# Optimization experiments

Hardware: AMD Instinct MI355X
Metric: run time of the kernel (lower is better)

## Reference

```python
import jax, jax.numpy as jnp
import numpy as np

N, D, H, E = 50000, 128, 512, 500000

def setup_inputs() -> dict:
    key = jax.random.key(0)
    k1, k2, k3, k4 = jax.random.split(key, 4)
    z = jax.random.normal(k1, (N, D), dtype=jnp.float32)
    edge_index = jax.random.randint(k2, (2, E), 0, N, dtype=jnp.int64)
    # torch Linear weights: fc1 [H, 2D], fc2 [1, H]
    W1 = jax.random.normal(k3, (H, 2 * D), dtype=jnp.float32) * (1.0 / np.sqrt(2 * D))
    b1 = jnp.zeros((H,), dtype=jnp.float32)
    W2 = jax.random.normal(k4, (1, H), dtype=jnp.float32) * (1.0 / np.sqrt(H))
    b2 = jnp.zeros((1,), dtype=jnp.float32)
    return {"z": z, "edge_index": edge_index, "W1": W1, "b1": b1, "W2": W2, "b2": b2}

def reference(z, edge_index, W1, b1, W2, b2):
    # gather endpoints and concat along feature dim: [E, 2D]
    z_cat = jnp.concatenate([z[edge_index[0]], z[edge_index[1]]], axis=1)
    # dropout is identity at eval (drop_rate effectively 0 for the baseline)
    h = jax.nn.relu(jnp.einsum('ef,hf->eh', z_cat, W1) + b1)  # [E, H]
    y = (jnp.einsum('eh,oh->eo', h, W2) + b2).reshape(-1)     # [E]
    return y
```

## Files before the change

kernel.cpp:

```cpp
#include <hip/hip_runtime.h>


typedef __bf16 bf16x8 __attribute__((ext_vector_type(8)));
typedef float f32x4  __attribute__((ext_vector_type(4)));
typedef float f32x16 __attribute__((ext_vector_type(16)));

__device__ __forceinline__ unsigned short f2b(float f) {
    unsigned int u = __float_as_uint(f);
    u = (u + 0x7fffu + ((u >> 16) & 1u)) >> 16;
    return (unsigned short)u;
}

__device__ __forceinline__ void gload_lds16(const unsigned short* g, unsigned short* l) {
    __builtin_amdgcn_global_load_lds(
        (const __attribute__((address_space(1))) unsigned int*)g,
        (__attribute__((address_space(3))) unsigned int*)l, 16, 0, 0);
}

__global__ void prep_kernel(const float* __restrict__ z, const float* __restrict__ W1,
                            const float* __restrict__ b2p,
                            unsigned short* __restrict__ zb, unsigned short* __restrict__ w1s,
                            float* __restrict__ outz, int nz4, int nout4) {
    int stride = gridDim.x * blockDim.x;
    const int nw = 256 * 64;
    const int total = nz4 + nw + nout4;
    const float b2v = b2p[0];
    for (int idx = blockIdx.x * blockDim.x + threadIdx.x; idx < total; idx += stride) {
        if (idx < nz4) {
            float4 v = ((const float4*)z)[idx];
            ushort4 o;
            o.x = f2b(v.x); o.y = f2b(v.y); o.z = f2b(v.z); o.w = f2b(v.w);
            ((ushort4*)zb)[idx] = o;
        } else if (idx < nz4 + nw) {
            int u = idx - nz4;
            int lane = u & 63;
            int blk  = u >> 6;
            int h  = (blk >> 4) * 32 + (lane & 31);
            int kb = (blk & 15) * 16 + (lane >> 5) * 8;
            const float* src = W1 + h * 256 + kb;
            ushort4 o0, o1;
            float4 v0 = *(const float4*)(src);
            float4 v1 = *(const float4*)(src + 4);
            o0.x = f2b(v0.x); o0.y = f2b(v0.y); o0.z = f2b(v0.z); o0.w = f2b(v0.w);
            o1.x = f2b(v1.x); o1.y = f2b(v1.y); o1.z = f2b(v1.z); o1.w = f2b(v1.w);
            ushort4* dst = (ushort4*)(w1s + u * 8);
            dst[0] = o0; dst[1] = o1;
        } else {
            ((float4*)outz)[idx - nz4 - nw] = (float4){b2v, b2v, b2v, b2v};
        }
    }
}

__global__ __launch_bounds__(512, 2)
void edge_mlp_kernel(const int* __restrict__ ei, const unsigned short* __restrict__ zb,
                     const unsigned short* __restrict__ w1s,
                     const float* __restrict__ b1, const float* __restrict__ W2,
                     float* __restrict__ out, int E, int ntiles) {
    __shared__ unsigned short ldsA[2][64 * 256];
    __shared__ float ldsB1[512];
    __shared__ float ldsW2[512];

    const int tid  = threadIdx.x;
    const int lane = tid & 63;
    const int w    = tid >> 6;
    const int l31  = lane & 31;
    const int hi   = lane >> 5;
    const int G    = gridDim.x;
    const int t0   = blockIdx.x;
    if (t0 >= ntiles) return;

    ldsB1[tid] = b1[tid];
    ldsW2[tid] = W2[tid];

    uint4 breg[2][16];
    #pragma unroll
    for (int j = 0; j < 2; ++j)
        #pragma unroll
        for (int kst = 0; kst < 16; ++kst)
            breg[j][kst] = *(const uint4*)(w1s + (((w * 2 + j) * 16 + kst) << 9) + lane * 8);

    const int side = (lane >> 4) & 1;
    const int l15  = lane & 15;
    const int swz3 = (l31 & 7) << 3;

#define ISSUE_GATHER(BUF)                                                     \
    do {                                                                      \
        _Pragma("unroll")                                                     \
        for (int q_ = 0; q_ < 4; ++q_) {                                      \
            int m_   = w * 8 + q_ * 2 + hi;                                   \
            int s15_ = l15 ^ (m_ & 7);                                        \
            gload_lds16(zb + (((long)ival[q_]) << 7) + (s15_ << 3),           \
                        &ldsA[BUF][(w * 8 + q_ * 2) << 8]);                   \
        }                                                                     \
    } while (0)

    asm volatile("s_waitcnt vmcnt(0) lgkmcnt(0)" ::: "memory");

    int ival[4];
    #pragma unroll
    for (int q = 0; q < 4; ++q) {
        int e = t0 * 64 + w * 8 + q * 2 + hi;
        e = (e < E) ? e : (E - 1);
        ival[q] = ei[side * E + e];
    }
    ISSUE_GATHER(0);
    asm volatile("" ::: "memory");
    {
        int t1 = t0 + G;
        #pragma unroll
        for (int q = 0; q < 4; ++q) {
            int e = t1 * 64 + w * 8 + q * 2 + hi;
            e = (e < E) ? e : (E - 1);
            ival[q] = ei[side * E + e];
        }
    }
    asm volatile("" ::: "memory");
    if (hi == 0) {
        atomicAdd(&out[t0 * 64 + l31], 0.0f);
        atomicAdd(&out[t0 * 64 + 32 + l31], 0.0f);
    }

    int cur = 0;
    for (int t = t0; t < ntiles; t += G) {
        asm volatile("s_waitcnt vmcnt(6)" ::: "memory");
        __builtin_amdgcn_s_barrier();
        asm volatile("" ::: "memory");

        const unsigned short* bufc = &ldsA[cur][0];

        f32x16 acc[2][2];
        #pragma unroll
        for (int j = 0; j < 2; ++j)
            #pragma unroll
            for (int q = 0; q < 4; ++q) {
                f32x4 b = *(const f32x4*)&ldsB1[w * 64 + j * 32 + q * 8 + hi * 4];
                #pragma unroll
                for (int rr = 0; rr < 4; ++rr) {
                    acc[0][j][q * 4 + rr] = b[rr];
                    acc[1][j][q * 4 + rr] = b[rr];
                }
            }

        __builtin_amdgcn_s_setprio(1);
        #pragma unroll
        for (int kst = 0; kst < 8; ++kst) {
            bf16x8 a[2];
            #pragma unroll
            for (int i = 0; i < 2; ++i) {
                int s = kst * 2 + hi;
                int off = ((i * 32 + l31) << 8) + ((s & 16) << 3) + (((s & 15) << 3) ^ swz3);
                a[i] = *(const bf16x8*)&bufc[off];
            }
            #pragma unroll
            for (int i = 0; i < 2; ++i)
                #pragma unroll
                for (int j = 0; j < 2; ++j)
                    acc[i][j] = __builtin_amdgcn_mfma_f32_32x32x16_bf16(
                        *(const bf16x8*)&breg[j][kst], a[i], acc[i][j], 0, 0, 0);
        }
        __builtin_amdgcn_s_setprio(0);

        ISSUE_GATHER(cur ^ 1);
        asm volatile("" ::: "memory");

        __builtin_amdgcn_s_setprio(1);
        #pragma unroll
        for (int kst = 8; kst < 16; ++kst) {
            bf16x8 a[2];
            #pragma unroll
            for (int i = 0; i < 2; ++i) {
                int s = kst * 2 + hi;
                int off = ((i * 32 + l31) << 8) + ((s & 16) << 3) + (((s & 15) << 3) ^ swz3);
                a[i] = *(const bf16x8*)&bufc[off];
            }
            #pragma unroll
            for (int i = 0; i < 2; ++i)
                #pragma unroll
                for (int j = 0; j < 2; ++j)
                    acc[i][j] = __builtin_amdgcn_mfma_f32_32x32x16_bf16(
                        *(const bf16x8*)&breg[j][kst], a[i], acc[i][j], 0, 0, 0);
        }
        __builtin_amdgcn_s_setprio(0);

        {
            int tt = t + 2 * G;
            #pragma unroll
            for (int q = 0; q < 4; ++q) {
                int e = tt * 64 + w * 8 + q * 2 + hi;
                e = (e < E) ? e : (E - 1);
                ival[q] = ei[side * E + e];
            }
        }
        asm volatile("" ::: "memory");

        float s2[2];
        #pragma unroll
        for (int i = 0; i < 2; ++i) {
            float s = 0.f;
            #pragma unroll
            for (int j = 0; j < 2; ++j)
                #pragma unroll
                for (int q = 0; q < 4; ++q) {
                    f32x4 w2q = *(const f32x4*)&ldsW2[w * 64 + j * 32 + q * 8 + hi * 4];
                    #pragma unroll
                    for (int rr = 0; rr < 4; ++rr)
                        s = fmaf(fmaxf(acc[i][j][q * 4 + rr], 0.f), w2q[rr], s);
                }
            s += __shfl_xor(s, 32);
            s2[i] = s;
        }
        #pragma unroll
        for (int i = 0; i < 2; ++i) {
            int e = t * 64 + i * 32 + l31;
            if (hi == 0 && e < E) atomicAdd(&out[e], s2[i]);
        }

        cur ^= 1;
    }
#undef ISSUE_GATHER
}

extern "C" void kernel_launch(void* const* d_in, const int* in_sizes, int n_in,
                              void* d_out, int out_size, void* d_ws, size_t ws_size,
                              hipStream_t stream) {
    const float* z  = (const float*)d_in[0];
    const int*   ei = (const int*)d_in[1];
    const float* W1 = (const float*)d_in[2];
    const float* b1 = (const float*)d_in[3];
    const float* W2 = (const float*)d_in[4];
    const float* b2 = (const float*)d_in[5];
    float* out = (float*)d_out;

    const int E  = in_sizes[1] / 2;
    const int NZ = in_sizes[0];

    unsigned short* zb  = (unsigned short*)d_ws;
    unsigned short* w1s = zb + NZ;

    prep_kernel<<<2048, 256, 0, stream>>>(z, W1, b2, zb, w1s, out, NZ / 4, E / 4);

    const int ntiles = (E + 63) / 64;
    int grid = 256;
    edge_mlp_kernel<<<grid, 512, 0, stream>>>(ei, zb, w1s, b1, W2, out, E, ntiles);
}
```

Before: 190.5 us.

## Issue next-tile gather before MFMA loop and keep W2 in registers

Moves the gather of the next tile's rows and the index prefetch to the top of each iteration, right after the barrier, so they overlap the whole MFMA loop instead of only its second half. Holds W2 in registers instead of LDS. Zero-initialises the accumulators and adds b1 in the epilogue instead of seeding them with bias. This lengthens the time available to hide gather latency, at the cost of more register pressure. Issuing the gather into buffer cur^1 right after the barrier may also race with waves still reading that buffer from the previous iteration, since no second barrier protects it.

```diff
diff --git a/kernel.cpp b/kernel.cpp
--- a/kernel.cpp
+++ b/kernel.cpp
@@ -58,7 +58,6 @@
                      float* __restrict__ out, int E, int ntiles) {
     __shared__ unsigned short ldsA[2][64 * 256];
     __shared__ float ldsB1[512];
-    __shared__ float ldsW2[512];
 
     const int tid  = threadIdx.x;
     const int lane = tid & 63;
@@ -70,7 +69,6 @@
     if (t0 >= ntiles) return;
 
     ldsB1[tid] = b1[tid];
-    ldsW2[tid] = W2[tid];
 
     uint4 breg[2][16];
     #pragma unroll
@@ -78,6 +76,13 @@
         #pragma unroll
         for (int kst = 0; kst < 16; ++kst)
             breg[j][kst] = *(const uint4*)(w1s + (((w * 2 + j) * 16 + kst) << 9) + lane * 8);
+
+    f32x4 w2r[2][4];
+    #pragma unroll
+    for (int j = 0; j < 2; ++j)
+        #pragma unroll
+        for (int q = 0; q < 4; ++q)
+            w2r[j][q] = *(const f32x4*)&W2[w * 64 + j * 32 + q * 8 + hi * 4];
 
     const int side = (lane >> 4) & 1;
     const int l15  = lane & 15;
@@ -126,24 +131,32 @@
         __builtin_amdgcn_s_barrier();
         asm volatile("" ::: "memory");
 
+        ISSUE_GATHER(cur ^ 1);
+        asm volatile("" ::: "memory");
+        {
+            int tt = t + 2 * G;
+            #pragma unroll
+            for (int q = 0; q < 4; ++q) {
+                int e = tt * 64 + w * 8 + q * 2 + hi;
+                e = (e < E) ? e : (E - 1);
+                ival[q] = ei[side * E + e];
+            }
+        }
+        asm volatile("" ::: "memory");
+
         const unsigned short* bufc = &ldsA[cur][0];
 
         f32x16 acc[2][2];
         #pragma unroll
-        for (int j = 0; j < 2; ++j)
-            #pragma unroll
-            for (int q = 0; q < 4; ++q) {
-                f32x4 b = *(const f32x4*)&ldsB1[w * 64 + j * 32 + q * 8 + hi * 4];
+        for (int i = 0; i < 2; ++i)
+            #pragma unroll
+            for (int j = 0; j < 2; ++j)
                 #pragma unroll
-                for (int rr = 0; rr < 4; ++rr) {
-                    acc[0][j][q * 4 + rr] = b[rr];
-                    acc[1][j][q * 4 + rr] = b[rr];
-                }
-            }
+                for (int r = 0; r < 16; ++r) acc[i][j][r] = 0.f;
 
         __builtin_amdgcn_s_setprio(1);
         #pragma unroll
-        for (int kst = 0; kst < 8; ++kst) {
+        for (int kst = 0; kst < 16; ++kst) {
             bf16x8 a[2];
             #pragma unroll
             for (int i = 0; i < 2; ++i) {
@@ -160,39 +173,6 @@
         }
         __builtin_amdgcn_s_setprio(0);
 
-        ISSUE_GATHER(cur ^ 1);
-        asm volatile("" ::: "memory");
-
-        __builtin_amdgcn_s_setprio(1);
-        #pragma unroll
-        for (int kst = 8; kst < 16; ++kst) {
-            bf16x8 a[2];
-            #pragma unroll
-            for (int i = 0; i < 2; ++i) {
-                int s = kst * 2 + hi;
-                int off = ((i * 32 + l31) << 8) + ((s & 16) << 3) + (((s & 15) << 3) ^ swz3);
-                a[i] = *(const bf16x8*)&bufc[off];
-            }
-            #pragma unroll
-            for (int i = 0; i < 2; ++i)
-                #pragma unroll
-                for (int j = 0; j < 2; ++j)
-                    acc[i][j] = __builtin_amdgcn_mfma_f32_32x32x16_bf16(
-                        *(const bf16x8*)&breg[j][kst], a[i], acc[i][j], 0, 0, 0);
-        }
-        __builtin_amdgcn_s_setprio(0);
-
-        {
-            int tt = t + 2 * G;
-            #pragma unroll
-            for (int q = 0; q < 4; ++q) {
-                int e = tt * 64 + w * 8 + q * 2 + hi;
-                e = (e < E) ? e : (E - 1);
-                ival[q] = ei[side * E + e];
-            }
-        }
-        asm volatile("" ::: "memory");
-
         float s2[2];
         #pragma unroll
         for (int i = 0; i < 2; ++i) {
@@ -201,10 +181,11 @@
             for (int j = 0; j < 2; ++j)
                 #pragma unroll
                 for (int q = 0; q < 4; ++q) {
-                    f32x4 w2q = *(const f32x4*)&ldsW2[w * 64 + j * 32 + q * 8 + hi * 4];
+                    f32x4 b1q = *(const f32x4*)&ldsB1[w * 64 + j * 32 + q * 8 + hi * 4];
                     #pragma unroll
                     for (int rr = 0; rr < 4; ++rr)
-                        s = fmaf(fmaxf(acc[i][j][q * 4 + rr], 0.f), w2q[rr], s);
+                        s = fmaf(fmaxf(acc[i][j][q * 4 + rr] + b1q[rr], 0.f),
+                                 w2r[j][q][rr], s);
                 }
             s += __shfl_xor(s, 32);
             s2[i] = s;
```

Measured after the change: 220.7 us. +15.9%, slower.

## Deepen gather pipeline to four LDS buffers with two-tile unrolled loop

Applied to the files above, without the earlier changes.

Grows the LDS staging area from two to four edge-tile buffers. The main loop now processes two tiles per iteration, so gathers and index loads are issued two tiles ahead. The aim is to hide more latency on the random z-row gathers. The cost is doubling ldsA to 128 KB per block, which likely prevents two 512-thread blocks from sharing a CU and lowers occupancy. It also adds register pressure and wasted work on the padding tile when a block's tile count is odd.

```diff
diff --git a/kernel.cpp b/kernel.cpp
--- a/kernel.cpp
+++ b/kernel.cpp
@@ -56,7 +56,7 @@
                      const unsigned short* __restrict__ w1s,
                      const float* __restrict__ b1, const float* __restrict__ W2,
                      float* __restrict__ out, int E, int ntiles) {
-    __shared__ unsigned short ldsA[2][64 * 256];
+    __shared__ unsigned short ldsA[4][64 * 256];
     __shared__ float ldsB1[512];
     __shared__ float ldsW2[512];
 
@@ -83,141 +83,217 @@
     const int l15  = lane & 15;
     const int swz3 = (l31 & 7) << 3;
 
-#define ISSUE_GATHER(BUF)                                                     \
+#define ISSUE_GATHER(BUF, IV)                                                 \
     do {                                                                      \
         _Pragma("unroll")                                                     \
         for (int q_ = 0; q_ < 4; ++q_) {                                      \
             int m_   = w * 8 + q_ * 2 + hi;                                   \
             int s15_ = l15 ^ (m_ & 7);                                        \
-            gload_lds16(zb + (((long)ival[q_]) << 7) + (s15_ << 3),           \
+            gload_lds16(zb + (((long)(IV)[q_]) << 7) + (s15_ << 3),           \
                         &ldsA[BUF][(w * 8 + q_ * 2) << 8]);                   \
         }                                                                     \
     } while (0)
 
+#define LOAD_IDX(IV, T)                                                       \
+    do {                                                                      \
+        _Pragma("unroll")                                                     \
+        for (int q_ = 0; q_ < 4; ++q_) {                                      \
+            int e_ = (T) * 64 + w * 8 + q_ * 2 + hi;                          \
+            e_ = (e_ < E) ? e_ : (E - 1);                                     \
+            (IV)[q_] = ei[side * E + e_];                                     \
+        }                                                                     \
+    } while (0)
+
     asm volatile("s_waitcnt vmcnt(0) lgkmcnt(0)" ::: "memory");
 
-    int ival[4];
-    #pragma unroll
-    for (int q = 0; q < 4; ++q) {
-        int e = t0 * 64 + w * 8 + q * 2 + hi;
-        e = (e < E) ? e : (E - 1);
-        ival[q] = ei[side * E + e];
-    }
-    ISSUE_GATHER(0);
+    int ivalA[4], ivalB[4];
+    LOAD_IDX(ivalA, t0);
+    LOAD_IDX(ivalB, t0 + G);
+    ISSUE_GATHER(0, ivalA);
+    ISSUE_GATHER(1, ivalB);
     asm volatile("" ::: "memory");
-    {
-        int t1 = t0 + G;
-        #pragma unroll
-        for (int q = 0; q < 4; ++q) {
-            int e = t1 * 64 + w * 8 + q * 2 + hi;
-            e = (e < E) ? e : (E - 1);
-            ival[q] = ei[side * E + e];
-        }
-    }
+    LOAD_IDX(ivalA, t0 + 2 * G);
+    LOAD_IDX(ivalB, t0 + 3 * G);
     asm volatile("" ::: "memory");
     if (hi == 0) {
         atomicAdd(&out[t0 * 64 + l31], 0.0f);
         atomicAdd(&out[t0 * 64 + 32 + l31], 0.0f);
     }
 
-    int cur = 0;
-    for (int t = t0; t < ntiles; t += G) {
-        asm volatile("s_waitcnt vmcnt(6)" ::: "memory");
+    int p = 0;
+    for (int t = t0; t < ntiles; t += 2 * G) {
+        asm volatile("s_waitcnt vmcnt(10)" ::: "memory");
         __builtin_amdgcn_s_barrier();
         asm volatile("" ::: "memory");
 
-        const unsigned short* bufc = &ldsA[cur][0];
-
-        f32x16 acc[2][2];
-        #pragma unroll
-        for (int j = 0; j < 2; ++j)
-            #pragma unroll
-            for (int q = 0; q < 4; ++q) {
-                f32x4 b = *(const f32x4*)&ldsB1[w * 64 + j * 32 + q * 8 + hi * 4];
-                #pragma unroll
-                for (int rr = 0; rr < 4; ++rr) {
-                    acc[0][j][q * 4 + rr] = b[rr];
-                    acc[1][j][q * 4 + rr] = b[rr];
-                }
-            }
-
-        __builtin_amdgcn_s_setprio(1);
-        #pragma unroll
-        for (int kst = 0; kst < 8; ++kst) {
-            bf16x8 a[2];
+        const int nb = p ^ 2;
+
+        {
+            const unsigned short* bufc = &ldsA[p][0];
+            f32x16 acc[2][2];
+            #pragma unroll
+            for (int j = 0; j < 2; ++j)
+                #pragma unroll
+                for (int q = 0; q < 4; ++q) {
+                    f32x4 b = *(const f32x4*)&ldsB1[w * 64 + j * 32 + q * 8 + hi * 4];
+                    #pragma unroll
+                    for (int rr = 0; rr < 4; ++rr) {
+                        acc[0][j][q * 4 + rr] = b[rr];
+                        acc[1][j][q * 4 + rr] = b[rr];
+                    }
+                }
+
+            __builtin_amdgcn_s_setprio(1);
+            #pragma unroll
+            for (int kst = 0; kst < 8; ++kst) {
+                bf16x8 a[2];
+                #pragma unroll
+                for (int i = 0; i < 2; ++i) {
+                    int s = kst * 2 + hi;
+                    int off = ((i * 32 + l31) << 8) + ((s & 16) << 3) + (((s & 15) << 3) ^ swz3);
+                    a[i] = *(const bf16x8*)&bufc[off];
+                }
+                #pragma unroll
+                for (int i = 0; i < 2; ++i)
+                    #pragma unroll
+                    for (int j = 0; j < 2; ++j)
+                        acc[i][j] = __builtin_amdgcn_mfma_f32_32x32x16_bf16(
+                            *(const bf16x8*)&breg[j][kst], a[i], acc[i][j], 0, 0, 0);
+            }
+            __builtin_amdgcn_s_setprio(0);
+
+            ISSUE_GATHER(nb, ivalA);
+            asm volatile("" ::: "memory");
+
+            __builtin_amdgcn_s_setprio(1);
+            #pragma unroll
+            for (int kst = 8; kst < 16; ++kst) {
+                bf16x8 a[2];
+                #pragma unroll
+                for (int i = 0; i < 2; ++i) {
+                    int s = kst * 2 + hi;
+                    int off = ((i * 32 + l31) << 8) + ((s & 16) << 3) + (((s & 15) << 3) ^ swz3);
+                    a[i] = *(const bf16x8*)&bufc[off];
+                }
+                #pragma unroll
+                for (int i = 0; i < 2; ++i)
+                    #pragma unroll
+                    for (int j = 0; j < 2; ++j)
+                        acc[i][j] = __builtin_amdgcn_mfma_f32_32x32x16_bf16(
+                            *(const bf16x8*)&breg[j][kst], a[i], acc[i][j], 0, 0, 0);
+            }
+            __builtin_amdgcn_s_setprio(0);
+
+            float s2[2];
             #pragma unroll
             for (int i = 0; i < 2; ++i) {
-                int s = kst * 2 + hi;
-                int off = ((i * 32 + l31) << 8) + ((s & 16) << 3) + (((s & 15) << 3) ^ swz3);
-                a[i] = *(const bf16x8*)&bufc[off];
-            }
-            #pragma unroll
-            for (int i = 0; i < 2; ++i)
+                float s = 0.f;
                 #pragma unroll
                 for (int j = 0; j < 2; ++j)
-                    acc[i][j] = __builtin_amdgcn_mfma_f32_32x32x16_bf16(
-                        *(const bf16x8*)&breg[j][kst], a[i], acc[i][j], 0, 0, 0);
+                    #pragma unroll
+                    for (int q = 0; q < 4; ++q) {
+                        f32x4 w2q = *(const f32x4*)&ldsW2[w * 64 + j * 32 + q * 8 + hi * 4];
+                        #pragma unroll
+                        for (int rr = 0; rr < 4; ++rr)
+                            s = fmaf(fmaxf(acc[i][j][q * 4 + rr], 0.f), w2q[rr], s);
+                    }
+                s += __shfl_xor(s, 32);
+                s2[i] = s;
+            }
+            #pragma unroll
+            for (int i = 0; i < 2; ++i) {
+                int e = t * 64 + i * 32 + l31;
+                if (hi == 0 && e < E) atomicAdd(&out[e], s2[i]);
+            }
         }
-        __builtin_amdgcn_s_setprio(0);
-
-        ISSUE_GATHER(cur ^ 1);
-        asm volatile("" ::: "memory");
-
-        __builtin_amdgcn_s_setprio(1);
-        #pragma unroll
-        for (int kst = 8; kst < 16; ++kst) {
-            bf16x8 a[2];
+
+        {
+            const int tB = t + G;
+            const unsigned short* bufc = &ldsA[p + 1][0];
+            f32x16 acc[2][2];
+            #pragma unroll
+            for (int j = 0; j < 2; ++j)
+                #pragma unroll
+                for (int q = 0; q < 4; ++q) {
+                    f32x4 b = *(const f32x4*)&ldsB1[w * 64 + j * 32 + q * 8 + hi * 4];
+                    #pragma unroll
+                    for (int rr = 0; rr < 4; ++rr) {
+                        acc[0][j][q * 4 + rr] = b[rr];
+                        acc[1][j][q * 4 + rr] = b[rr];
+                    }
+                }
+
+            __builtin_amdgcn_s_setprio(1);
+            #pragma unroll
+            for (int kst = 0; kst < 8; ++kst) {
+                bf16x8 a[2];
+                #pragma unroll
+                for (int i = 0; i < 2; ++i) {
+                    int s = kst * 2 + hi;
+                    int off = ((i * 32 + l31) << 8) + ((s & 16) << 3) + (((s & 15) << 3) ^ swz3);
+                    a[i] = *(const bf16x8*)&bufc[off];
+                }
+                #pragma unroll
+                for (int i = 0; i < 2; ++i)
+                    #pragma unroll
+                    for (int j = 0; j < 2; ++j)
+                        acc[i][j] = __builtin_amdgcn_mfma_f32_32x32x16_bf16(
+                            *(const bf16x8*)&breg[j][kst], a[i], acc[i][j], 0, 0, 0);
+            }
+            __builtin_amdgcn_s_setprio(0);
+
+            ISSUE_GATHER(nb + 1, ivalB);
+            asm volatile("" ::: "memory");
+            LOAD_IDX(ivalA, t + 4 * G);
+            LOAD_IDX(ivalB, t + 5 * G);
+            asm volatile("" ::: "memory");
+
+            __builtin_amdgcn_s_setprio(1);
+            #pragma unroll
+            for (int kst = 8; kst < 16; ++kst) {
+                bf16x8 a[2];
+                #pragma unroll
+                for (int i = 0; i < 2; ++i) {
+                    int s = kst * 2 + hi;
+                    int off = ((i * 32 + l31) << 8) + ((s & 16) << 3) + (((s & 15) << 3) ^ swz3);
+                    a[i] = *(const bf16x8*)&bufc[off];
+                }
+                #pragma unroll
+                for (int i = 0; i < 2; ++i)
+                    #pragma unroll
+                    for (int j = 0; j < 2; ++j)
+                        acc[i][j] = __builtin_amdgcn_mfma_f32_32x32x16_bf16(
+                            *(const bf16x8*)&breg[j][kst], a[i], acc[i][j], 0, 0, 0);
+            }
+            __builtin_amdgcn_s_setprio(0);
+
+            float s2[2];
             #pragma unroll
             for (int i = 0; i < 2; ++i) {
-                int s = kst * 2 + hi;
-                int off = ((i * 32 + l31) << 8) + ((s & 16) << 3) + (((s & 15) << 3) ^ swz3);
-                a[i] = *(const bf16x8*)&bufc[off];
-            }
-            #pragma unroll
-            for (int i = 0; i < 2; ++i)
+                float s = 0.f;
                 #pragma unroll
                 for (int j = 0; j < 2; ++j)
-                    acc[i][j] = __builtin_amdgcn_mfma_f32_32x32x16_bf16(
-                        *(const bf16x8*)&breg[j][kst], a[i], acc[i][j], 0, 0, 0);
+                    #pragma unroll
+                    for (int q = 0; q < 4; ++q) {
+                        f32x4 w2q = *(const f32x4*)&ldsW2[w * 64 + j * 32 + q * 8 + hi * 4];
+                        #pragma unroll
+                        for (int rr = 0; rr < 4; ++rr)
+                            s = fmaf(fmaxf(acc[i][j][q * 4 + rr], 0.f), w2q[rr], s);
+                    }
+                s += __shfl_xor(s, 32);
+                s2[i] = s;
+            }
+            #pragma unroll
+            for (int i = 0; i < 2; ++i) {
+                int e = tB * 64 + i * 32 + l31;
+                if (hi == 0 && e < E) atomicAdd(&out[e], s2[i]);
+            }
         }
-        __builtin_amdgcn_s_setprio(0);
-
-        {
-            int tt = t + 2 * G;
-            #pragma unroll
-            for (int q = 0; q < 4; ++q) {
-                int e = tt * 64 + w * 8 + q * 2 + hi;
-                e = (e < E) ? e : (E - 1);
-                ival[q] = ei[side * E + e];
-            }
-        }
-        asm volatile("" ::: "memory");
-
-        float s2[2];
-        #pragma unroll
-        for (int i = 0; i < 2; ++i) {
-            float s = 0.f;
-            #pragma unroll
-            for (int j = 0; j < 2; ++j)
-                #pragma unroll
-                for (int q = 0; q < 4; ++q) {
-                    f32x4 w2q = *(const f32x4*)&ldsW2[w * 64 + j * 32 + q * 8 + hi * 4];
-                    #pragma unroll
-                    for (int rr = 0; rr < 4; ++rr)
-                        s = fmaf(fmaxf(acc[i][j][q * 4 + rr], 0.f), w2q[rr], s);
-                }
-            s += __shfl_xor(s, 32);
-            s2[i] = s;
-        }
-        #pragma unroll
-        for (int i = 0; i < 2; ++i) {
-            int e = t * 64 + i * 32 + l31;
-            if (hi == 0 && e < E) atomicAdd(&out[e], s2[i]);
-        }
-
-        cur ^= 1;
+
+        p ^= 2;
     }
 #undef ISSUE_GATHER
+#undef LOAD_IDX
 }
 
 extern "C" void kernel_launch(void* const* d_in, const int* in_sizes, int n_in,
```

New measurement: 206.1 us. +8.2%, slower.
